# Kernel tuning notes

Measured on AMD Instinct MI355X. Metric: run time of the kernel, lower is better.

The kernel has to match this reference:

```python
import jax, jax.numpy as jnp
import numpy as np

NODES_PER_GRAPH = 21
NUM_GRAPHS = 50000
N = NODES_PER_GRAPH * NUM_GRAPHS  # 1,050,000 nodes
NUM_FEATURES = 3
NUM_CLASSES = 29
H1, H2 = 64, 128
BN_EPS = 1e-5

_HAND = np.array([(0, 1), (1, 2), (2, 3), (3, 4), (0, 5), (5, 6), (6, 7), (7, 8),
                  (0, 9), (9, 10), (10, 11), (11, 12), (0, 13), (13, 14), (14, 15),
                  (15, 16), (0, 17), (17, 18), (18, 19), (19, 20)], dtype=np.int64).T  # [2,20]


def setup_inputs() -> dict:
    key = jax.random.key(0)
    ks = jax.random.split(key, 16)
    # Tile hand skeleton across NUM_GRAPHS disjoint graphs with node offsets.
    offsets = (np.arange(NUM_GRAPHS, dtype=np.int64) * NODES_PER_GRAPH)  # [G]
    ei = (_HAND[:, None, :] + offsets[None, :, None]).reshape(2, -1)      # [2, G*20]
    edge_index = jnp.asarray(ei)
    batch = jnp.asarray(np.repeat(np.arange(NUM_GRAPHS, dtype=np.int64), NODES_PER_GRAPH))

    x = jax.random.normal(ks[0], (N, NUM_FEATURES), dtype=jnp.float32)

    def lin(k, fi, fo):
        kw, kb = jax.random.split(k)
        s = 1.0 / np.sqrt(fi)
        return (jax.random.uniform(kw, (fi, fo), jnp.float32, -s, s),
                jax.random.uniform(kb, (fo,), jnp.float32, -s, s))

    W1, b1 = lin(ks[1], NUM_FEATURES, H1)
    W2, b2 = lin(ks[2], H1, H2)
    W3, b3 = lin(ks[3], H2, NUM_CLASSES)

    def bn(k, d):
        k1, k2, k3, k4 = jax.random.split(k, 4)
        return (1.0 + 0.1 * jax.random.normal(k1, (d,), jnp.float32),   # gamma
                0.1 * jax.random.normal(k2, (d,), jnp.float32),          # beta
                0.01 * jax.random.normal(k3, (d,), jnp.float32),         # running_mean
                jax.random.uniform(k4, (d,), jnp.float32, 0.5, 1.5))     # running_var

    g1, be1, m1, v1 = bn(ks[4], H1)
    g2, be2, m2, v2 = bn(ks[5], H2)

    return {"x": x, "W1": W1, "b1": b1, "g1": g1, "be1": be1, "m1": m1, "v1": v1,
            "W2": W2, "b2": b2, "g2": g2, "be2": be2, "m2": m2, "v2": v2,
            "W3": W3, "b3": b3, "edge_index": edge_index, "batch": batch}


def gcn_conv(x, W, b, src, dst):
    """PyG GCNConv: linear, add self-loops, sym-normalized scatter-add, bias."""
    h = x @ W                                              # [N, Fout]
    deg = jnp.zeros((N,), x.dtype).at[dst].add(1.0) + 1.0  # in-degree incl. self-loop
    dinv = deg ** -0.5
    msg = h[src] * (dinv[src] * dinv[dst])[:, None]        # edge-wise gather + normalize
    out = jnp.zeros_like(h).at[dst].add(msg)               # scatter-add aggregation
    out = out + h * (dinv * dinv)[:, None]                 # self-loop contribution
    return out + b


def bn_eval(x, gamma, beta, mean, var):
    return (x - mean) * (gamma * jax.lax.rsqrt(var + BN_EPS)) + beta


def reference(x, W1, b1, g1, be1, m1, v1, W2, b2, g2, be2, m2, v2, W3, b3,
              edge_index, batch):
    src, dst = edge_index[0], edge_index[1]
    h = jax.nn.relu(bn_eval(gcn_conv(x, W1, b1, src, dst), g1, be1, m1, v1))
    # dropout is identity in eval mode
    h = jax.nn.relu(bn_eval(gcn_conv(h, W2, b2, src, dst), g2, be2, m2, v2))
    h = gcn_conv(h, W3, b3, src, dst)                      # [N, C]
    summed = jax.ops.segment_sum(h, batch, num_segments=NUM_GRAPHS)
    counts = jax.ops.segment_sum(jnp.ones((N,), h.dtype), batch, num_segments=NUM_GRAPHS)
    pooled = summed / counts[:, None]                      # global mean pool [G, C]
    return jax.nn.log_softmax(pooled, axis=1)
```

## Files before the change

### kernel.cpp

```cpp
#include <hip/hip_runtime.h>
#include <math.h>


#define G_TOTAL 50000
#define GPB 4
#define NBLK (G_TOTAL / GPB)
#define NCLS 29
#define BN_EPS 1e-5f
#define INV_SQRT2 0.70710678118654752440f
#define ROOT_W 0.21597780504441608f

#define WS_W1B  0
#define WS_B2   256
#define WS_B3   384
#define WS_W3T  416
#define WS_BF   4128
#define WS_TOTAL (WS_BF + 4096)

#define TSTRIDE 1056

typedef short s16x8 __attribute__((ext_vector_type(8)));
typedef float f32x4 __attribute__((ext_vector_type(4)));

__device__ __forceinline__ unsigned f2bf_rne(float f) {
    unsigned u = __float_as_uint(f);
    return (u + 0x7FFFu + ((u >> 16) & 1u)) >> 16;
}

__global__ void prep_kernel(const float* __restrict__ W1, const float* __restrict__ b1,
                            const float* __restrict__ g1, const float* __restrict__ be1,
                            const float* __restrict__ m1, const float* __restrict__ v1,
                            const float* __restrict__ W2, const float* __restrict__ b2,
                            const float* __restrict__ g2, const float* __restrict__ be2,
                            const float* __restrict__ m2, const float* __restrict__ v2,
                            const float* __restrict__ W3, const float* __restrict__ b3,
                            float* __restrict__ ws) {
    int t = blockIdx.x * blockDim.x + threadIdx.x;
    if (t < 256) {
        int k = t >> 2, comp = t & 3;
        float s = g1[k] * rsqrtf(v1[k] + BN_EPS);
        float v;
        if (comp < 3) v = W1[comp * 64 + k] * s;
        else          v = (b1[k] - m1[k]) * s + be1[k];
        ws[WS_W1B + t] = v;
    } else if (t < 384) {
        int j = t - 256;
        float s = g2[j] * rsqrtf(v2[j] + BN_EPS);
        ws[WS_B2 + j] = (b2[j] - m2[j]) * s + be2[j];
    } else if (t < 416) {
        int j = t - 384;
        ws[WS_B3 + j] = (j < NCLS) ? b3[j] : 0.f;
    } else if (t < WS_BF) {
        int i = t - WS_W3T;
        if (i < 3712) {
            int c = i >> 7, k = i & 127;
            ws[WS_W3T + i] = W3[k * NCLS + c];
        }
    } else if (t < WS_TOTAL) {
        int i = t - WS_BF;
        int d  = i & 3;
        int l  = (i >> 2) & 63;
        int ss = (i >> 8) & 1;
        int n  = i >> 9;
        int kg = l >> 4, r = l & 15;
        int c = 16 * n + r;
        float sc = g2[c] * rsqrtf(v2[c] + BN_EPS);
        int k0 = 32 * ss + 8 * kg + 2 * d;
        unsigned h0 = f2bf_rne(W2[k0 * 128 + c] * sc);
        unsigned h1 = f2bf_rne(W2[(k0 + 1) * 128 + c] * sc);
        ((unsigned*)ws)[WS_BF + i] = (h1 << 16) | h0;
    }
}

__global__ __launch_bounds__(256, 8)
void gcn_main(const float* __restrict__ x, const float* __restrict__ ws,
              float* __restrict__ out) {
    __shared__ __align__(16) char sFrag[12 * TSTRIDE];
    __shared__ __align__(16) float4 sW1B[64];
    __shared__ __align__(16) float sPX[512];

    const int tid = threadIdx.x;
    const long long blk = blockIdx.x;

    if (tid < 64) sW1B[tid] = ((const float4*)ws)[tid];
    if (tid < 63) ((float4*)sPX)[tid] = ((const float4*)(x + blk * 252))[tid];
    if (tid >= 64 && tid < 64 + 132)
        *(float4*)(sFrag + 10 * TSTRIDE + (tid - 64) * 16) =
            make_float4(0.f, 0.f, 0.f, 0.f);
    __syncthreads();

    if (tid < 168) {
        const int node = tid >> 1;
        const int s = tid & 1;
        const int k0 = s * 32;
        const int g4 = (node * 3121) >> 16;
        const int p  = node - 21 * g4;
        const int dist  = (p == 0) ? 0 : (((p & 3) == 1) ? p : 1);
        const float cw  = ((p & 3) == 1) ? INV_SQRT2 : 0.5f;
        const int jp = p - dist;
        const int dist2 = (jp == 0) ? 0 : (((jp & 3) == 1) ? jp : 1);
        const float cw2 = ((jp & 3) == 1) ? INV_SQRT2 : 0.5f;

        const float* xs = (const float*)sPX + node * 3;
        const float* xq = xs - dist * 3;
        const float* xg = xq - dist2 * 3;
        const float ax0 = fmaf(cw,  xq[0], 0.5f * xs[0]);
        const float ax1 = fmaf(cw,  xq[1], 0.5f * xs[1]);
        const float ax2 = fmaf(cw,  xq[2], 0.5f * xs[2]);
        const float bx0 = fmaf(cw2, xg[0], 0.5f * xq[0]);
        const float bx1 = fmaf(cw2, xg[1], 0.5f * xq[1]);
        const float bx2 = fmaf(cw2, xg[2], 0.5f * xq[2]);

        float az[32];
        #pragma unroll
        for (int kk = 0; kk < 32; ++kk) {
            const float4 wv = sW1B[k0 + kk];
            float ts = fmaf(ax0, wv.x, wv.w);
            ts = fmaf(ax1, wv.y, ts);
            ts = fmaf(ax2, wv.z, ts);
            ts = fmaxf(ts, 0.f);
            float tp = fmaf(bx0, wv.x, wv.w);
            tp = fmaf(bx1, wv.y, tp);
            tp = fmaf(bx2, wv.z, tp);
            tp = fmaxf(tp, 0.f);
            az[kk] = fmaf(cw, tp, 0.5f * ts);
        }
        unsigned dw[16];
        #pragma unroll
        for (int q = 0; q < 16; ++q)
            dw[q] = __builtin_amdgcn_perm(__float_as_uint(az[2*q+1]),
                                          __float_as_uint(az[2*q]), 0x07060302u);
        char* fragB = sFrag + ((p >> 2) * 2 + s) * TSTRIDE + (4 * g4 + (p & 3)) * 16;
        #pragma unroll
        for (int kg = 0; kg < 4; ++kg)
            *(uint4*)(fragB + kg * 256) =
                make_uint4(dw[4*kg], dw[4*kg+1], dw[4*kg+2], dw[4*kg+3]);
    }
    __syncthreads();

    {
        const int w = tid >> 6;
        const int lane = tid & 63;
        const int r = lane & 15;
        const int lg = lane >> 4;
        const uint4* wsB = (const uint4*)((const unsigned*)ws + WS_BF);
        const uint4 B00 = wsB[((2*w+0)*2 + 0)*64 + lane];
        const uint4 B01 = wsB[((2*w+0)*2 + 1)*64 + lane];
        const uint4 B10 = wsB[((2*w+1)*2 + 0)*64 + lane];
        const uint4 B11 = wsB[((2*w+1)*2 + 1)*64 + lane];
        const float b2c0 = ws[WS_B2 + 32*w + r];
        const float b2c1 = ws[WS_B2 + 32*w + 16 + r];
        const char* fragA = sFrag + lane * 16;

        float pg0 = 0.f, pg1 = 0.f;
        #pragma unroll
        for (int m = 0; m < 6; ++m) {
            const s16x8 A0 = *(const s16x8*)(fragA + (2*m + 0) * TSTRIDE);
            const s16x8 A1 = *(const s16x8*)(fragA + (2*m + 1) * TSTRIDE);
            f32x4 acc0 = {0.f, 0.f, 0.f, 0.f};
            f32x4 acc1 = {0.f, 0.f, 0.f, 0.f};
            acc0 = __builtin_amdgcn_mfma_f32_16x16x32_bf16(A0, *(const s16x8*)&B00, acc0, 0, 0, 0);
            acc0 = __builtin_amdgcn_mfma_f32_16x16x32_bf16(A1, *(const s16x8*)&B01, acc0, 0, 0, 0);
            acc1 = __builtin_amdgcn_mfma_f32_16x16x32_bf16(A0, *(const s16x8*)&B10, acc1, 0, 0, 0);
            acc1 = __builtin_amdgcn_mfma_f32_16x16x32_bf16(A1, *(const s16x8*)&B11, acc1, 0, 0, 0);

            #pragma unroll
            for (int i = 0; i < 4; ++i) {
                const int p = 4*m + i;
                if (p < 21) {
                    const float wgt = (p == 0) ? ROOT_W
                                    : (((p & 3) == 0) ? (0.5f / 21.f) : (1.f / 21.f));
                    pg0 = fmaf(wgt, fmaxf(acc0[i] + b2c0, 0.f), pg0);
                    pg1 = fmaf(wgt, fmaxf(acc1[i] + b2c1, 0.f), pg1);
                }
            }
        }
        sPX[lg * 128 + 32*w + r]      = pg0;
        sPX[lg * 128 + 32*w + 16 + r] = pg1;
    }
    __syncthreads();

    float* sLg = (float*)sFrag;
    if (tid < GPB * NCLS) {
        const int g = (tid * 2260) >> 16;
        const int c = tid - g * NCLS;
        const float4* w3 = (const float4*)(ws + WS_W3T + c * 128);
        const float4* pp = (const float4*)&sPX[g * 128];
        float acc3 = ws[WS_B3 + c];
        #pragma unroll
        for (int k = 0; k < 32; ++k) {
            const float4 wv = w3[k];
            const float4 pv = pp[k];
            acc3 = fmaf(pv.x, wv.x, acc3);
            acc3 = fmaf(pv.y, wv.y, acc3);
            acc3 = fmaf(pv.z, wv.z, acc3);
            acc3 = fmaf(pv.w, wv.w, acc3);
        }
        sLg[tid] = acc3;
    }
    __syncthreads();

    if (tid < 128) {
        const int g = tid >> 5, c = tid & 31;
        const bool act = (c < NCLS);
        float v = act ? sLg[g * NCLS + c] : -1e30f;
        float m = v;
        m = fmaxf(m, __shfl_xor(m, 1));
        m = fmaxf(m, __shfl_xor(m, 2));
        m = fmaxf(m, __shfl_xor(m, 4));
        m = fmaxf(m, __shfl_xor(m, 8));
        m = fmaxf(m, __shfl_xor(m, 16));
        float e = act ? __expf(v - m) : 0.f;
        float ss = e;
        ss += __shfl_xor(ss, 1);
        ss += __shfl_xor(ss, 2);
        ss += __shfl_xor(ss, 4);
        ss += __shfl_xor(ss, 8);
        ss += __shfl_xor(ss, 16);
        if (act)
            out[blk * (GPB * NCLS) + g * NCLS + c] = v - m - __logf(ss);
    }
}

extern "C" void kernel_launch(void* const* d_in, const int* in_sizes, int n_in,
                              void* d_out, int out_size, void* d_ws, size_t ws_size,
                              hipStream_t stream) {
    const float* x   = (const float*)d_in[0];
    const float* W1  = (const float*)d_in[1];
    const float* b1  = (const float*)d_in[2];
    const float* g1  = (const float*)d_in[3];
    const float* be1 = (const float*)d_in[4];
    const float* m1  = (const float*)d_in[5];
    const float* v1  = (const float*)d_in[6];
    const float* W2  = (const float*)d_in[7];
    const float* b2  = (const float*)d_in[8];
    const float* g2  = (const float*)d_in[9];
    const float* be2 = (const float*)d_in[10];
    const float* m2  = (const float*)d_in[11];
    const float* v2  = (const float*)d_in[12];
    const float* W3  = (const float*)d_in[13];
    const float* b3  = (const float*)d_in[14];
    float* out = (float*)d_out;
    float* ws  = (float*)d_ws;

    prep_kernel<<<(WS_TOTAL + 255) / 256, 256, 0, stream>>>(
        W1, b1, g1, be1, m1, v1, W2, b2, g2, be2, m2, v2, W3, b3, ws);

    gcn_main<<<NBLK, 256, 0, stream>>>(x, ws, out);
}
```

Baseline: 196.0 us.

## Process five graph chunks per block with double-buffered LDS pipeline

Each block now handles five 4-graph chunks instead of one. The MFMA phase of one chunk overlaps the layer-1 fragment build of the next through double-buffered LDS, and x is prefetched into registers two chunks ahead. The final linear layer and log-softmax are restructured so each wave handles one graph with a split-K dot product and wave-wide shuffles, which cuts barriers per chunk. The aim is to amortise B-fragment loads and launch overhead and to hide global latency, in exchange for lower occupancy (launch bounds 4) and a grid of only 2500 blocks.

```diff
diff --git a/kernel.cpp b/kernel.cpp
--- a/kernel.cpp
+++ b/kernel.cpp
@@ -4,7 +4,8 @@
 
 #define G_TOTAL 50000
 #define GPB 4
-#define NBLK (G_TOTAL / GPB)
+#define CPB 5
+#define NBLK (G_TOTAL / (GPB * CPB))
 #define NCLS 29
 #define BN_EPS 1e-5f
 #define INV_SQRT2 0.70710678118654752440f
@@ -18,6 +19,7 @@
 #define WS_TOTAL (WS_BF + 4096)
 
 #define TSTRIDE 1056
+#define FRAGBUF (12 * TSTRIDE)
 
 typedef short s16x8 __attribute__((ext_vector_type(8)));
 typedef float f32x4 __attribute__((ext_vector_type(4)));
@@ -72,153 +74,181 @@
     }
 }
 
-__global__ __launch_bounds__(256, 8)
+__global__ __launch_bounds__(256, 4)
 void gcn_main(const float* __restrict__ x, const float* __restrict__ ws,
               float* __restrict__ out) {
-    __shared__ __align__(16) char sFrag[12 * TSTRIDE];
+    __shared__ __align__(16) char sFrag[2][FRAGBUF];
     __shared__ __align__(16) float4 sW1B[64];
-    __shared__ __align__(16) float sPX[512];
+    __shared__ __align__(16) float4 sX[2][64];
+    __shared__ __align__(16) float sPool[4 * 132];
 
     const int tid = threadIdx.x;
-    const long long blk = blockIdx.x;
+    const int lane = tid & 63;
+    const int w = tid >> 6;
+    const int r = lane & 15;
+    const int lg = lane >> 4;
+    const long long cbase = (long long)blockIdx.x * CPB;
+
+    const uint4* wsB = (const uint4*)((const unsigned*)ws + WS_BF);
+    const uint4 B00 = wsB[((2*w+0)*2 + 0)*64 + lane];
+    const uint4 B01 = wsB[((2*w+0)*2 + 1)*64 + lane];
+    const uint4 B10 = wsB[((2*w+1)*2 + 0)*64 + lane];
+    const uint4 B11 = wsB[((2*w+1)*2 + 1)*64 + lane];
+    const float b2c0 = ws[WS_B2 + 32*w + r];
+    const float b2c1 = ws[WS_B2 + 32*w + 16 + r];
+    const int cc = lane >> 1;
+    const int h3 = lane & 1;
+    const float b3r = ws[WS_B3 + (cc < NCLS ? cc : 0)];
+    const float* w3base = ws + WS_W3T + cc * 128 + 64 * h3;
+
+    auto phase1 = [&](int buf) {
+        if (tid < 168) {
+            const int node = tid >> 1;
+            const int s = tid & 1;
+            const int k0q = s * 32;
+            const int g4 = (node * 3121) >> 16;
+            const int p  = node - 21 * g4;
+            const int dist  = (p == 0) ? 0 : (((p & 3) == 1) ? p : 1);
+            const float cw  = ((p & 3) == 1) ? INV_SQRT2 : 0.5f;
+            const int jp = p - dist;
+            const int dist2 = (jp == 0) ? 0 : (((jp & 3) == 1) ? jp : 1);
+            const float cw2 = ((jp & 3) == 1) ? INV_SQRT2 : 0.5f;
+            const float* xs = (const float*)&sX[buf][0] + node * 3;
+            const float* xq = xs - dist * 3;
+            const float* xg = xq - dist2 * 3;
+            const float ax0 = fmaf(cw,  xq[0], 0.5f * xs[0]);
+            const float ax1 = fmaf(cw,  xq[1], 0.5f * xs[1]);
+            const float ax2 = fmaf(cw,  xq[2], 0.5f * xs[2]);
+            const float bx0 = fmaf(cw2, xg[0], 0.5f * xq[0]);
+            const float bx1 = fmaf(cw2, xg[1], 0.5f * xq[1]);
+            const float bx2 = fmaf(cw2, xg[2], 0.5f * xq[2]);
+            char* fragW = sFrag[buf] + ((p >> 2) * 2 + s) * TSTRIDE
+                        + (4 * g4 + (p & 3)) * 16;
+            #pragma unroll
+            for (int q = 0; q < 4; ++q) {
+                unsigned dws[4];
+                #pragma unroll
+                for (int pr = 0; pr < 4; ++pr) {
+                    float azv[2];
+                    #pragma unroll
+                    for (int e = 0; e < 2; ++e) {
+                        const float4 wv = sW1B[k0q + q*8 + pr*2 + e];
+                        float ts = fmaf(ax0, wv.x, wv.w);
+                        ts = fmaf(ax1, wv.y, ts);
+                        ts = fmaf(ax2, wv.z, ts);
+                        ts = fmaxf(ts, 0.f);
+                        float tp = fmaf(bx0, wv.x, wv.w);
+                        tp = fmaf(bx1, wv.y, tp);
+                        tp = fmaf(bx2, wv.z, tp);
+                        tp = fmaxf(tp, 0.f);
+                        azv[e] = fmaf(cw, tp, 0.5f * ts);
+                    }
+                    dws[pr] = __builtin_amdgcn_perm(__float_as_uint(azv[1]),
+                                                    __float_as_uint(azv[0]),
+                                                    0x07060302u);
+                }
+                *(uint4*)(fragW + q * 256) =
+                    make_uint4(dws[0], dws[1], dws[2], dws[3]);
+            }
+        }
+    };
 
     if (tid < 64) sW1B[tid] = ((const float4*)ws)[tid];
-    if (tid < 63) ((float4*)sPX)[tid] = ((const float4*)(x + blk * 252))[tid];
-    if (tid >= 64 && tid < 64 + 132)
-        *(float4*)(sFrag + 10 * TSTRIDE + (tid - 64) * 16) =
+    #pragma unroll
+    for (int i = tid; i < 264; i += 256) {
+        const int b = (i >= 132) ? 1 : 0;
+        const int off = i - b * 132;
+        *(float4*)(sFrag[b] + 10 * TSTRIDE + off * 16) =
             make_float4(0.f, 0.f, 0.f, 0.f);
+    }
+    float4 xr0, xr1, xreg;
+    if (tid < 63) {
+        xr0  = ((const float4*)(x + cbase * 252))[tid];
+        xr1  = ((const float4*)(x + (cbase + 1) * 252))[tid];
+        xreg = ((const float4*)(x + (cbase + 2) * 252))[tid];
+        sX[0][tid] = xr0;
+    }
     __syncthreads();
-
-    if (tid < 168) {
-        const int node = tid >> 1;
-        const int s = tid & 1;
-        const int k0 = s * 32;
-        const int g4 = (node * 3121) >> 16;
-        const int p  = node - 21 * g4;
-        const int dist  = (p == 0) ? 0 : (((p & 3) == 1) ? p : 1);
-        const float cw  = ((p & 3) == 1) ? INV_SQRT2 : 0.5f;
-        const int jp = p - dist;
-        const int dist2 = (jp == 0) ? 0 : (((jp & 3) == 1) ? jp : 1);
-        const float cw2 = ((jp & 3) == 1) ? INV_SQRT2 : 0.5f;
-
-        const float* xs = (const float*)sPX + node * 3;
-        const float* xq = xs - dist * 3;
-        const float* xg = xq - dist2 * 3;
-        const float ax0 = fmaf(cw,  xq[0], 0.5f * xs[0]);
-        const float ax1 = fmaf(cw,  xq[1], 0.5f * xs[1]);
-        const float ax2 = fmaf(cw,  xq[2], 0.5f * xs[2]);
-        const float bx0 = fmaf(cw2, xg[0], 0.5f * xq[0]);
-        const float bx1 = fmaf(cw2, xg[1], 0.5f * xq[1]);
-        const float bx2 = fmaf(cw2, xg[2], 0.5f * xq[2]);
-
-        float az[32];
-        #pragma unroll
-        for (int kk = 0; kk < 32; ++kk) {
-            const float4 wv = sW1B[k0 + kk];
-            float ts = fmaf(ax0, wv.x, wv.w);
-            ts = fmaf(ax1, wv.y, ts);
-            ts = fmaf(ax2, wv.z, ts);
-            ts = fmaxf(ts, 0.f);
-            float tp = fmaf(bx0, wv.x, wv.w);
-            tp = fmaf(bx1, wv.y, tp);
-            tp = fmaf(bx2, wv.z, tp);
-            tp = fmaxf(tp, 0.f);
-            az[kk] = fmaf(cw, tp, 0.5f * ts);
-        }
-        unsigned dw[16];
-        #pragma unroll
-        for (int q = 0; q < 16; ++q)
-            dw[q] = __builtin_amdgcn_perm(__float_as_uint(az[2*q+1]),
-                                          __float_as_uint(az[2*q]), 0x07060302u);
-        char* fragB = sFrag + ((p >> 2) * 2 + s) * TSTRIDE + (4 * g4 + (p & 3)) * 16;
-        #pragma unroll
-        for (int kg = 0; kg < 4; ++kg)
-            *(uint4*)(fragB + kg * 256) =
-                make_uint4(dw[4*kg], dw[4*kg+1], dw[4*kg+2], dw[4*kg+3]);
-    }
+    phase1(0);
+    if (tid < 63) sX[1][tid] = xr1;
     __syncthreads();
 
-    {
-        const int w = tid >> 6;
-        const int lane = tid & 63;
-        const int r = lane & 15;
-        const int lg = lane >> 4;
-        const uint4* wsB = (const uint4*)((const unsigned*)ws + WS_BF);
-        const uint4 B00 = wsB[((2*w+0)*2 + 0)*64 + lane];
-        const uint4 B01 = wsB[((2*w+0)*2 + 1)*64 + lane];
-        const uint4 B10 = wsB[((2*w+1)*2 + 0)*64 + lane];
-        const uint4 B11 = wsB[((2*w+1)*2 + 1)*64 + lane];
-        const float b2c0 = ws[WS_B2 + 32*w + r];
-        const float b2c1 = ws[WS_B2 + 32*w + 16 + r];
-        const char* fragA = sFrag + lane * 16;
-
-        float pg0 = 0.f, pg1 = 0.f;
-        #pragma unroll
-        for (int m = 0; m < 6; ++m) {
-            const s16x8 A0 = *(const s16x8*)(fragA + (2*m + 0) * TSTRIDE);
-            const s16x8 A1 = *(const s16x8*)(fragA + (2*m + 1) * TSTRIDE);
-            f32x4 acc0 = {0.f, 0.f, 0.f, 0.f};
-            f32x4 acc1 = {0.f, 0.f, 0.f, 0.f};
-            acc0 = __builtin_amdgcn_mfma_f32_16x16x32_bf16(A0, *(const s16x8*)&B00, acc0, 0, 0, 0);
-            acc0 = __builtin_amdgcn_mfma_f32_16x16x32_bf16(A1, *(const s16x8*)&B01, acc0, 0, 0, 0);
-            acc1 = __builtin_amdgcn_mfma_f32_16x16x32_bf16(A0, *(const s16x8*)&B10, acc1, 0, 0, 0);
-            acc1 = __builtin_amdgcn_mfma_f32_16x16x32_bf16(A1, *(const s16x8*)&B11, acc1, 0, 0, 0);
-
+    for (int ck = 0; ck < CPB; ++ck) {
+        const int cur = ck & 1;
+
+        {
+            const char* fragA = sFrag[cur] + lane * 16;
+            float pg0 = 0.f, pg1 = 0.f;
             #pragma unroll
-            for (int i = 0; i < 4; ++i) {
-                const int p = 4*m + i;
-                if (p < 21) {
-                    const float wgt = (p == 0) ? ROOT_W
-                                    : (((p & 3) == 0) ? (0.5f / 21.f) : (1.f / 21.f));
-                    pg0 = fmaf(wgt, fmaxf(acc0[i] + b2c0, 0.f), pg0);
-                    pg1 = fmaf(wgt, fmaxf(acc1[i] + b2c1, 0.f), pg1);
+            for (int m = 0; m < 6; ++m) {
+                const s16x8 A0 = *(const s16x8*)(fragA + (2*m + 0) * TSTRIDE);
+                const s16x8 A1 = *(const s16x8*)(fragA + (2*m + 1) * TSTRIDE);
+                f32x4 acc0 = {0.f, 0.f, 0.f, 0.f};
+                f32x4 acc1 = {0.f, 0.f, 0.f, 0.f};
+                acc0 = __builtin_amdgcn_mfma_f32_16x16x32_bf16(A0, *(const s16x8*)&B00, acc0, 0, 0, 0);
+                acc0 = __builtin_amdgcn_mfma_f32_16x16x32_bf16(A1, *(const s16x8*)&B01, acc0, 0, 0, 0);
+                acc1 = __builtin_amdgcn_mfma_f32_16x16x32_bf16(A0, *(const s16x8*)&B10, acc1, 0, 0, 0);
+                acc1 = __builtin_amdgcn_mfma_f32_16x16x32_bf16(A1, *(const s16x8*)&B11, acc1, 0, 0, 0);
+                #pragma unroll
+                for (int i = 0; i < 4; ++i) {
+                    const int p = 4*m + i;
+                    if (p < 21) {
+                        const float wgt = (p == 0) ? ROOT_W
+                                        : (((p & 3) == 0) ? (0.5f / 21.f) : (1.f / 21.f));
+                        pg0 = fmaf(wgt, fmaxf(acc0[i] + b2c0, 0.f), pg0);
+                        pg1 = fmaf(wgt, fmaxf(acc1[i] + b2c1, 0.f), pg1);
+                    }
                 }
             }
-        }
-        sPX[lg * 128 + 32*w + r]      = pg0;
-        sPX[lg * 128 + 32*w + 16 + r] = pg1;
-    }
-    __syncthreads();
-
-    float* sLg = (float*)sFrag;
-    if (tid < GPB * NCLS) {
-        const int g = (tid * 2260) >> 16;
-        const int c = tid - g * NCLS;
-        const float4* w3 = (const float4*)(ws + WS_W3T + c * 128);
-        const float4* pp = (const float4*)&sPX[g * 128];
-        float acc3 = ws[WS_B3 + c];
-        #pragma unroll
-        for (int k = 0; k < 32; ++k) {
-            const float4 wv = w3[k];
-            const float4 pv = pp[k];
-            acc3 = fmaf(pv.x, wv.x, acc3);
-            acc3 = fmaf(pv.y, wv.y, acc3);
-            acc3 = fmaf(pv.z, wv.z, acc3);
-            acc3 = fmaf(pv.w, wv.w, acc3);
-        }
-        sLg[tid] = acc3;
-    }
-    __syncthreads();
-
-    if (tid < 128) {
-        const int g = tid >> 5, c = tid & 31;
-        const bool act = (c < NCLS);
-        float v = act ? sLg[g * NCLS + c] : -1e30f;
-        float m = v;
-        m = fmaxf(m, __shfl_xor(m, 1));
-        m = fmaxf(m, __shfl_xor(m, 2));
-        m = fmaxf(m, __shfl_xor(m, 4));
-        m = fmaxf(m, __shfl_xor(m, 8));
-        m = fmaxf(m, __shfl_xor(m, 16));
-        float e = act ? __expf(v - m) : 0.f;
-        float ss = e;
-        ss += __shfl_xor(ss, 1);
-        ss += __shfl_xor(ss, 2);
-        ss += __shfl_xor(ss, 4);
-        ss += __shfl_xor(ss, 8);
-        ss += __shfl_xor(ss, 16);
-        if (act)
-            out[blk * (GPB * NCLS) + g * NCLS + c] = v - m - __logf(ss);
+            sPool[lg * 132 + 32*w + r]      = pg0;
+            sPool[lg * 132 + 32*w + 16 + r] = pg1;
+
+            if (ck < CPB - 1) phase1(cur ^ 1);
+        }
+        __syncthreads();
+
+        {
+            float v = -1e30f;
+            if (lane < 2 * NCLS) {
+                const float4* pp = (const float4*)&sPool[w * 132 + 64 * h3];
+                const float4* w3 = (const float4*)w3base;
+                float acc3 = 0.f;
+                #pragma unroll
+                for (int q = 0; q < 16; ++q) {
+                    const float4 pv = pp[q];
+                    const float4 wv = w3[q];
+                    acc3 = fmaf(pv.x, wv.x, acc3);
+                    acc3 = fmaf(pv.y, wv.y, acc3);
+                    acc3 = fmaf(pv.z, wv.z, acc3);
+                    acc3 = fmaf(pv.w, wv.w, acc3);
+                }
+                v = acc3;
+            }
+            v += __shfl_xor(v, 1);
+            if (lane < 2 * NCLS) v += b3r;
+            float m = v;
+            m = fmaxf(m, __shfl_xor(m, 2));
+            m = fmaxf(m, __shfl_xor(m, 4));
+            m = fmaxf(m, __shfl_xor(m, 8));
+            m = fmaxf(m, __shfl_xor(m, 16));
+            m = fmaxf(m, __shfl_xor(m, 32));
+            float e = (lane < 2 * NCLS) ? __expf(v - m) : 0.f;
+            float ss = e;
+            ss += __shfl_xor(ss, 2);
+            ss += __shfl_xor(ss, 4);
+            ss += __shfl_xor(ss, 8);
+            ss += __shfl_xor(ss, 16);
+            ss += __shfl_xor(ss, 32);
+            if (h3 == 0 && lane < 2 * NCLS)
+                out[((cbase + ck) * GPB + w) * NCLS + cc] = v - m - __logf(ss);
+
+            if (tid < 63) {
+                if (ck <= CPB - 3) sX[cur][tid] = xreg;
+                if (ck <= CPB - 4)
+                    xreg = ((const float4*)(x + (cbase + ck + 3) * 252))[tid];
+            }
+        }
+        __syncthreads();
     }
 }
 
```

Measured after the change: 187.6 us. 4.3% less time.
